# Performance work log

Hardware: AMD Instinct MI355X
Metric: run time of the kernel (lower is better)

Reference implementation:

```python
import jax, jax.numpy as jnp
import numpy as np

K = 128      # num_topics
T = 256      # num_times
E = 320      # rho_size
H = 10       # num_heads (fixed in source)
HD = E // H  # head dim
TM1 = T - 1
EPS = 1e-5   # nn.LayerNorm default eps


def setup_inputs() -> dict:
    key = jax.random.key(0)
    ks = jax.random.split(key, 6)
    s = 0.02
    return {
        "mu_0_alpha": jax.random.normal(ks[0], (1, K, E), jnp.float32),
        "qkv_w": jax.random.normal(ks[1], (3 * E, E), jnp.float32) * s,
        "qkv_b": jnp.zeros((3 * E,), jnp.float32),
        "in_proj_w": jax.random.normal(ks[2], (3 * E, E), jnp.float32) * s,
        "in_proj_b": jnp.zeros((3 * E,), jnp.float32),
        "out_w": jax.random.normal(ks[3], (E, E), jnp.float32) * s,
        "out_b": jnp.zeros((E,), jnp.float32),
        "ln_g": jnp.ones((E,), jnp.float32),
        "ln_b": jnp.zeros((E,), jnp.float32),
    }


def _layer_norm(x, g, b):
    m = jnp.mean(x, axis=-1, keepdims=True)
    v = jnp.mean((x - m) ** 2, axis=-1, keepdims=True)
    return (x - m) * jax.lax.rsqrt(v + EPS) * g + b


def reference(mu_0_alpha, qkv_w, qkv_b, in_proj_w, in_proj_b, out_w, out_b, ln_g, ln_b):
    # nn.MultiheadAttention in-projection split (q/k/v same embed_dim)
    Wq, Wk, Wv = jnp.split(in_proj_w, 3, axis=0)   # each (E, E)
    bq, bk, bv = jnp.split(in_proj_b, 3, axis=0)
    scale = 1.0 / np.sqrt(HD)

    alpha0 = _layer_norm(mu_0_alpha[0], ln_g, ln_b)  # (K, E)
    kc0 = jnp.zeros((TM1 * K, E), jnp.float32)       # persistent projected-K cache
    vc0 = jnp.zeros((TM1 * K, E), jnp.float32)
    pos = jnp.arange(TM1 * K)

    def step(carry, idx):
        alpha, kc, vc = carry
        # per-step qkv_proj (the module's own Linear, before MHA's in-proj)
        qkv = alpha @ qkv_w.T + qkv_b                 # (K, 3E)
        q, k, v = jnp.split(qkv, 3, axis=-1)
        # MHA in-projections; store projected K/V in the cache (equivalent to
        # projecting the concatenated cache each step, since proj is per-row)
        q2 = (q @ Wq.T + bq) * scale                  # (K, E)
        k2 = k @ Wk.T + bk
        v2 = v @ Wv.T + bv
        kc = jax.lax.dynamic_update_slice(kc, k2, (idx * K, 0))
        vc = jax.lax.dynamic_update_slice(vc, v2, (idx * K, 0))
        qh = q2.reshape(K, H, HD).transpose(1, 0, 2)          # (H, K, HD)
        kh = kc.reshape(TM1 * K, H, HD).transpose(1, 0, 2)    # (H, S, HD)
        vh = vc.reshape(TM1 * K, H, HD).transpose(1, 0, 2)
        scores = jnp.einsum('hqd,hkd->hqk', qh, kh)           # (H, K, S)
        valid = pos < (idx + 1) * K                            # growing-KV mask
        scores = jnp.where(valid[None, None, :], scores, -1e30)
        w = jax.nn.softmax(scores, axis=-1)
        o = jnp.einsum('hqk,hkd->hqd', w, vh)                  # (H, K, HD)
        o = o.transpose(1, 0, 2).reshape(K, E) @ out_w.T + out_b
        new_alpha = _layer_norm(o + alpha, ln_g, ln_b)         # residual + LN
        return (new_alpha, kc, vc), new_alpha

    _, alphas_rest = jax.lax.scan(step, (alpha0, kc0, vc0), jnp.arange(TM1))
    return jnp.concatenate([alpha0[None], alphas_rest], axis=0)  # (T, K, E)
```

## Files before the change

kernel.cpp:

```cpp
#include <hip/hip_runtime.h>
#include <hip/hip_bf16.h>
#include <math.h>

typedef __hip_bfloat16 bf16;
using short4v = __attribute__((ext_vector_type(4))) short;
using short8 = __attribute__((ext_vector_type(8))) short;
using f32x4  = __attribute__((ext_vector_type(4))) float;

#define E_ 320
#define K_ 128
#define H_ 10
#define HD_ 32
#define T_ 256
#define TM1_ 255
#define SMAX_ (TM1_*K_)
#define MAXCH_ 30
#define QSCALE 0.17677669529663687f
#define EPS_LN 1e-5f

__device__ __forceinline__ float ldin(const void* p, size_t i, int isbf){
  if (isbf) return __bfloat162float(((const bf16*)p)[i]);
  return ((const float*)p)[i];
}
__device__ __forceinline__ void stout(void* p, size_t i, float v, int isbf){
  if (isbf) ((bf16*)p)[i] = __float2bfloat16(v);
  else      ((float*)p)[i] = v;
}

__device__ __forceinline__ void reduce2_320(float& a, float& b, float* sc){
  #pragma unroll
  for (int off = 32; off > 0; off >>= 1){
    a += __shfl_down(a, off, 64);
    b += __shfl_down(b, off, 64);
  }
  int w = threadIdx.x >> 6, lane = threadIdx.x & 63;
  __syncthreads();
  if (lane == 0){ sc[w] = a; sc[8+w] = b; }
  __syncthreads();
  a = sc[0]+sc[1]+sc[2]+sc[3]+sc[4];
  b = sc[8]+sc[9]+sc[10]+sc[11]+sc[12];
}

__global__ void detect_kernel(const void* __restrict__ mu0, int* __restrict__ flag){
  int lane = threadIdx.x;
  const unsigned short* u = (const unsigned short*)mu0;
  int cnt = 0;
  #pragma unroll
  for (int rep = 0; rep < 2; ++rep){
    unsigned short w = u[(size_t)(lane + rep*64) * 2];
    float v = __uint_as_float(((unsigned int)w) << 16);
    float a = fabsf(v);
    if (a >= 1e-4f && a <= 64.f) cnt++;
  }
  #pragma unroll
  for (int off = 32; off > 0; off >>= 1) cnt += __shfl_down(cnt, off, 64);
  if (lane == 0) *flag = (cnt >= 64) ? 1 : 0;
}

__global__ __launch_bounds__(256) void setup_wc(const void* __restrict__ inw,
                                                const void* __restrict__ qkvw,
                                                bf16* __restrict__ WcB,
                                                const int* __restrict__ flagp){
  const int isbf = *flagp;
  int sec = blockIdx.z;
  int i = blockIdx.y*16 + threadIdx.y;
  int o = blockIdx.x*16 + threadIdx.x;
  __shared__ float As[16][17];
  __shared__ float Bs[16][17];
  float acc = 0.f;
  for (int mt = 0; mt < E_; mt += 16){
    As[threadIdx.y][threadIdx.x] = ldin(inw, ((size_t)(sec*E_ + blockIdx.x*16 + threadIdx.x))*E_ + mt + threadIdx.y, isbf);
    Bs[threadIdx.y][threadIdx.x] = ldin(qkvw, ((size_t)(sec*E_ + mt + threadIdx.x))*E_ + blockIdx.y*16 + threadIdx.y, isbf);
    __syncthreads();
    #pragma unroll
    for (int mm = 0; mm < 16; ++mm) acc += Bs[threadIdx.y][mm] * As[mm][threadIdx.x];
    __syncthreads();
  }
  if (sec == 0) acc *= QSCALE;
  WcB[((size_t)(sec*E_ + o))*E_ + i] = __float2bfloat16(acc);
}

__global__ __launch_bounds__(256) void setup_misc(const void* __restrict__ inw,
                                                  const void* __restrict__ inb,
                                                  const void* __restrict__ qkvb,
                                                  const void* __restrict__ outw,
                                                  const void* __restrict__ outb,
                                                  const void* __restrict__ lng,
                                                  const void* __restrict__ lnb,
                                                  float* __restrict__ bc,
                                                  bf16* __restrict__ owB,
                                                  float* __restrict__ vec,
                                                  const int* __restrict__ flagp){
  const int isbf = *flagp;
  int id = blockIdx.x*256 + threadIdx.x;
  if (id < 960){
    int sec = id / E_, o = id % E_;
    float acc = 0.f;
    for (int m = 0; m < E_; ++m)
      acc += ldin(inw, ((size_t)(sec*E_+o))*E_ + m, isbf) * ldin(qkvb, sec*E_ + m, isbf);
    acc += ldin(inb, id, isbf);
    if (sec == 0) acc *= QSCALE;
    bc[id] = acc;
  }
  int j = id - 1024;
  if (j >= 0 && j < E_*E_){
    owB[j] = __float2bfloat16(ldin(outw, j, isbf));
  }
  int v = id - (1024 + E_*E_);
  if (v >= 0 && v < 960){
    if (v < 320)       vec[v] = ldin(outb, v, isbf);
    else if (v < 640)  vec[v] = ldin(lng, v - 320, isbf);
    else               vec[v] = ldin(lnb, v - 640, isbf);
  }
}

__global__ __launch_bounds__(320) void ln0_kernel(const void* __restrict__ mu0,
                                                  const float* __restrict__ vec,
                                                  float* __restrict__ alpha,
                                                  void* __restrict__ out,
                                                  const int* __restrict__ flagp){
  const int isbf = *flagp;
  int r = blockIdx.x, c = threadIdx.x;
  __shared__ float sc[16];
  float x = ldin(mu0, (size_t)r*E_ + c, isbf);
  float s = x, s2 = x*x;
  reduce2_320(s, s2, sc);
  float mean = s * (1.f/E_);
  float var  = s2 * (1.f/E_) - mean*mean;
  float y = (x - mean) * rsqrtf(var + EPS_LN) * vec[320 + c] + vec[640 + c];
  alpha[(size_t)r*E_ + c] = y;
  stout(out, (size_t)r*E_ + c, y, isbf);
}

__global__ __launch_bounds__(512) void cp_kernel(const float* __restrict__ part,
                                                 const bf16* __restrict__ owB,
                                                 const bf16* __restrict__ WcB,
                                                 const float* __restrict__ bc,
                                                 const float* __restrict__ vec,
                                                 const float* __restrict__ ain,
                                                 float* __restrict__ aout,
                                                 void* __restrict__ out,
                                                 const int* __restrict__ flagp,
                                                 bf16* __restrict__ q2b,
                                                 bf16* __restrict__ kcb,
                                                 bf16* __restrict__ vtb,
                                                 int t, int nch, int do_combine, int do_project){
  const int isbf = *flagp;
  int cg = blockIdx.x;
  int rg = blockIdx.y;
  int r0 = rg*16;
  int tid = threadIdx.x;
  int w = tid >> 6, lane = tid & 63, cn = lane & 15, quad = lane >> 4;

  __shared__ bf16  af[16][328];
  __shared__ float xbuf[16][328];
  __shared__ bf16  a2[16][328];
  __shared__ float mlw[16][10][MAXCH_];
  __shared__ float mlL[16][10];

  if (do_combine){
    if (tid < 160){
      int r = tid / 10, h = tid % 10;
      float mst = -INFINITY;
      for (int ci = 0; ci < nch; ++ci)
        mst = fmaxf(mst, part[(((size_t)h*MAXCH_ + ci)*K_ + r0 + r)*36 + 32]);
      float L = 0.f;
      for (int ci = 0; ci < nch; ++ci){
        size_t base = (((size_t)h*MAXCH_ + ci)*K_ + r0 + r)*36;
        float wgt = __expf(part[base + 32] - mst);
        mlw[r][h][ci] = wgt;
        L += wgt * part[base + 33];
      }
      mlL[r][h] = L;
    }
    __syncthreads();
    for (int v = tid; v < 16*E_; v += 512){
      int r = v / E_, e = v % E_;
      int h = e >> 5, d = e & 31;
      float acc = 0.f;
      for (int ci = 0; ci < nch; ++ci)
        acc += mlw[r][h][ci] * part[(((size_t)h*MAXCH_ + ci)*K_ + r0 + r)*36 + d];
      af[r][e] = __float2bfloat16(acc / mlL[r][h]);
    }
    __syncthreads();

    {
      f32x4 acc[3]; int ntv[3]; int ntc = 0;
      for (int nt = w; nt < 20; nt += 8){ ntv[ntc] = nt; acc[ntc] = (f32x4){0.f,0.f,0.f,0.f}; ntc++; }
      for (int kk = 0; kk < 10; ++kk){
        short8 afr = *(const short8*)(const void*)(&af[cn][kk*32 + quad*8]);
        for (int i = 0; i < ntc; ++i){
          short8 bfr = *(const short8*)(const void*)(owB + ((size_t)(ntv[i]*16 + cn))*E_ + kk*32 + quad*8);
          acc[i] = __builtin_amdgcn_mfma_f32_16x16x32_bf16(afr, bfr, acc[i], 0, 0, 0);
        }
      }
      for (int i = 0; i < ntc; ++i){
        int col = ntv[i]*16 + cn;
        #pragma unroll
        for (int rr = 0; rr < 4; ++rr){
          int lr = quad*4 + rr;
          xbuf[lr][col] = acc[i][rr] + vec[col] + ain[(size_t)(r0+lr)*E_ + col];
        }
      }
    }
    __syncthreads();

    {
      int lr = tid >> 5;
      int j32 = tid & 31;
      float s = 0.f, s2 = 0.f;
      for (int c = j32; c < E_; c += 32){ float x = xbuf[lr][c]; s += x; s2 += x*x; }
      #pragma unroll
      for (int off = 1; off < 32; off <<= 1){
        s  += __shfl_xor(s, off, 32);
        s2 += __shfl_xor(s2, off, 32);
      }
      float mean = s * (1.f/E_);
      float var  = s2 * (1.f/E_) - mean*mean;
      float rs = rsqrtf(var + EPS_LN);
      for (int c = j32; c < E_; c += 32){
        float y = (xbuf[lr][c] - mean) * rs * vec[320 + c] + vec[640 + c];
        a2[lr][c] = __float2bfloat16(y);
        if (cg == 0){
          aout[(size_t)(r0+lr)*E_ + c] = y;
          stout(out, ((size_t)t*K_ + r0 + lr)*E_ + c, y, isbf);
        }
      }
    }
    __syncthreads();
  } else {
    for (int v = tid; v < 16*E_; v += 512){
      int r = v / E_, e = v % E_;
      a2[r][e] = __float2bfloat16(ain[(size_t)(r0+r)*E_ + e]);
    }
    __syncthreads();
  }

  if (!do_project) return;

  {
    f32x4 acc[3]; int ntv[3]; int ntc = 0;
    for (int nt = w; nt < 20; nt += 8){ ntv[ntc] = nt; acc[ntc] = (f32x4){0.f,0.f,0.f,0.f}; ntc++; }
    for (int kk = 0; kk < 10; ++kk){
      short8 afr = *(const short8*)(const void*)(&a2[cn][kk*32 + quad*8]);
      for (int i = 0; i < ntc; ++i){
        short8 bfr = *(const short8*)(const void*)(WcB + ((size_t)(cg*E_ + ntv[i]*16 + cn))*E_ + kk*32 + quad*8);
        acc[i] = __builtin_amdgcn_mfma_f32_16x16x32_bf16(afr, bfr, acc[i], 0, 0, 0);
      }
    }
    for (int i = 0; i < ntc; ++i){
      int coll = ntv[i]*16 + cn;
      float bias = bc[cg*E_ + coll];
      if (cg == 0){
        #pragma unroll
        for (int rr = 0; rr < 4; ++rr)
          q2b[(size_t)(r0 + quad*4 + rr)*E_ + coll] = __float2bfloat16(acc[i][rr] + bias);
      } else if (cg == 1){
        #pragma unroll
        for (int rr = 0; rr < 4; ++rr)
          kcb[((size_t)(t*K_ + r0 + quad*4 + rr))*E_ + coll] = __float2bfloat16(acc[i][rr] + bias);
      } else {
        union { short4v v; bf16 e[4]; } u;
        #pragma unroll
        for (int rr = 0; rr < 4; ++rr) u.e[rr] = __float2bfloat16(acc[i][rr] + bias);
        *(short4v*)(void*)(vtb + (size_t)coll*SMAX_ + t*K_ + r0 + quad*4) = u.v;
      }
    }
  }
}

__global__ __launch_bounds__(512) void attn_mfma(const bf16* __restrict__ q2b,
                                                 const bf16* __restrict__ kcb,
                                                 const bf16* __restrict__ vtb,
                                                 float* __restrict__ part,
                                                 int S, int chunkS){
  int ci = blockIdx.x, h = blockIdx.y;
  int w    = threadIdx.x >> 6;
  int lane = threadIdx.x & 63;
  int cn   = lane & 15;
  int quad = lane >> 4;
  __shared__ bf16 pbuf[8][16][40];

  int s0 = ci*chunkS, s1 = min(s0 + chunkS, S);

  short8 qf = *(const short8*)(const void*)(q2b + (size_t)(w*16 + cn)*E_ + h*HD_ + quad*8);

  f32x4 accT[2];
  accT[0] = (f32x4){0.f,0.f,0.f,0.f};
  accT[1] = (f32x4){0.f,0.f,0.f,0.f};
  float mcol = -INFINITY, lcol = 0.f;

  for (int sb = s0; sb < s1; sb += 32){
    short8 kf0 = *(const short8*)(const void*)(kcb + (size_t)(sb +      cn)*E_ + h*HD_ + quad*8);
    short8 kf1 = *(const short8*)(const void*)(kcb + (size_t)(sb + 16 + cn)*E_ + h*HD_ + quad*8);
    short8 vf0 = *(const short8*)(const void*)(vtb + (size_t)(h*HD_ +      cn)*SMAX_ + sb + quad*8);
    short8 vf1 = *(const short8*)(const void*)(vtb + (size_t)(h*HD_ + 16 + cn)*SMAX_ + sb + quad*8);
    f32x4 z = (f32x4){0.f,0.f,0.f,0.f};
    f32x4 sT0 = __builtin_amdgcn_mfma_f32_16x16x32_bf16(kf0, qf, z, 0, 0, 0);
    f32x4 sT1 = __builtin_amdgcn_mfma_f32_16x16x32_bf16(kf1, qf, z, 0, 0, 0);

    float mx = fmaxf(fmaxf(fmaxf(sT0[0], sT0[1]), fmaxf(sT0[2], sT0[3])),
                     fmaxf(fmaxf(sT1[0], sT1[1]), fmaxf(sT1[2], sT1[3])));
    mx = fmaxf(mx, __shfl_xor(mx, 16, 64));
    mx = fmaxf(mx, __shfl_xor(mx, 32, 64));
    float mn = fmaxf(mcol, mx);
    float corr = __expf(mcol - mn);
    mcol = mn;

    float p0[4], p1[4];
    #pragma unroll
    for (int r = 0; r < 4; ++r){ p0[r] = __expf(sT0[r] - mn); p1[r] = __expf(sT1[r] - mn); }
    float ps = (p0[0]+p0[1]) + (p0[2]+p0[3]) + (p1[0]+p1[1]) + (p1[2]+p1[3]);
    ps += __shfl_xor(ps, 16, 64);
    ps += __shfl_xor(ps, 32, 64);
    lcol = lcol*corr + ps;
    accT[0] *= corr;
    accT[1] *= corr;

    union { short4v v; bf16 e[4]; } u0, u1;
    #pragma unroll
    for (int r = 0; r < 4; ++r){ u0.e[r] = __float2bfloat16(p0[r]); u1.e[r] = __float2bfloat16(p1[r]); }
    *(short4v*)(void*)(&pbuf[w][cn][quad*4])      = u0.v;
    *(short4v*)(void*)(&pbuf[w][cn][16 + quad*4]) = u1.v;
    asm volatile("s_waitcnt lgkmcnt(0)" ::: "memory");
    short8 pf = *(const short8*)(const void*)(&pbuf[w][cn][quad*8]);
    accT[0] = __builtin_amdgcn_mfma_f32_16x16x32_bf16(vf0, pf, accT[0], 0, 0, 0);
    accT[1] = __builtin_amdgcn_mfma_f32_16x16x32_bf16(vf1, pf, accT[1], 0, 0, 0);
  }

  size_t base = (((size_t)h*MAXCH_ + ci)*K_ + 16*w + cn)*36;
  *(f32x4*)(part + base + quad*4)      = accT[0];
  *(f32x4*)(part + base + 16 + quad*4) = accT[1];
  if (quad == 0){ part[base + 32] = mcol; part[base + 33] = lcol; }
}

extern "C" void kernel_launch(void* const* d_in, const int* in_sizes, int n_in,
                              void* d_out, int out_size, void* d_ws, size_t ws_size,
                              hipStream_t stream){
  const void* mu0  = d_in[0];
  const void* qkvw = d_in[1];
  const void* qkvb = d_in[2];
  const void* inw  = d_in[3];
  const void* inb  = d_in[4];
  const void* outw = d_in[5];
  const void* outb = d_in[6];
  const void* lng  = d_in[7];
  const void* lnb  = d_in[8];
  float* ws = (float*)d_ws;

  const size_t O_WCB    = 0;
  const size_t O_OWB    = 153600;
  const size_t O_BC     = 204800;
  const size_t O_VEC    = 205824;
  const size_t O_ALPHA0 = 206848;
  const size_t O_ALPHA1 = 247808;
  const size_t O_PART   = 288768;
  const size_t O_FLAG   = 1671168;
  const size_t O_Q2     = 1671200;
  const size_t O_KC     = 1691680;
  const size_t O_VT     = 6914080;

  bf16*  WcB   = (bf16*)(ws + O_WCB);
  bf16*  owB   = (bf16*)(ws + O_OWB);
  float* bc    = ws + O_BC;
  float* vec   = ws + O_VEC;
  float* abuf0 = ws + O_ALPHA0;
  float* abuf1 = ws + O_ALPHA1;
  float* part  = ws + O_PART;
  int*   flag  = (int*)(ws + O_FLAG);
  bf16*  q2b   = (bf16*)(ws + O_Q2);
  bf16*  kcb   = (bf16*)(ws + O_KC);
  bf16*  vtb   = (bf16*)(ws + O_VT);

  detect_kernel<<<dim3(1), dim3(64), 0, stream>>>(mu0, flag);
  setup_wc<<<dim3(20,20,3), dim3(16,16), 0, stream>>>(inw, qkvw, WcB, flag);
  setup_misc<<<dim3(408), dim3(256), 0, stream>>>(inw, inb, qkvb, outw, outb, lng, lnb, bc, owB, vec, flag);
  ln0_kernel<<<dim3(128), dim3(320), 0, stream>>>(mu0, vec, abuf0, d_out, flag);

  int nch_prev = 0;
  for (int t = 0; t < TM1_; ++t){
    float* ain  = (t == 0) ? abuf0 : ((t & 1) ? abuf0 : abuf1);
    float* aout = (t & 1) ? abuf1 : abuf0;
    cp_kernel<<<dim3(3,8), dim3(512), 0, stream>>>(part, owB, WcB, bc, vec, ain, aout,
                                                   d_out, flag, q2b, kcb, vtb,
                                                   t, nch_prev, (t > 0) ? 1 : 0, 1);
    int S = (t+1)*K_;
    int nch = (S + 255) / 256; if (nch > MAXCH_) nch = MAXCH_;
    int chunkS = (((S + nch - 1)/nch) + 127) / 128 * 128;
    int nchU = (S + chunkS - 1) / chunkS;
    attn_mfma<<<dim3(nchU, H_), dim3(512), 0, stream>>>(q2b, kcb, vtb, part, S, chunkS);
    nch_prev = nchU;
  }
  {
    int t = TM1_;
    float* ain  = (t & 1) ? abuf0 : abuf1;
    float* aout = (t & 1) ? abuf1 : abuf0;
    cp_kernel<<<dim3(3,8), dim3(512), 0, stream>>>(part, owB, WcB, bc, vec, ain, aout,
                                                   d_out, flag, q2b, kcb, vtb,
                                                   t, nch_prev, 1, 0);
  }
}
```

Before: 21.46 ms.

## Fuse per-step kernels into one persistent kernel with grid barriers

Replaces the roughly 510 per-timestep kernel launches (cp_kernel plus attn_mfma) with one persistent kernel of 256 blocks that loops over timesteps and separates phases with a software grid-wide atomic barrier. Attention chunking is retuned to finer 32-aligned chunks capped at 25, and the combine step is unrolled with multiple accumulators. Shared memory is aliased across phases to cut its footprint. The goal is to remove launch overhead and improve parallelism. It relies on all 256 blocks being co-resident and adds the cost of the barrier spin.

```diff
diff --git a/kernel.cpp b/kernel.cpp
--- a/kernel.cpp
+++ b/kernel.cpp
@@ -14,7 +14,8 @@
 #define T_ 256
 #define TM1_ 255
 #define SMAX_ (TM1_*K_)
-#define MAXCH_ 30
+#define MAXCH_ 25
+#define NBLK_ 256
 #define QSCALE 0.17677669529663687f
 #define EPS_LN 1e-5f
 
@@ -41,7 +42,8 @@
   b = sc[8]+sc[9]+sc[10]+sc[11]+sc[12];
 }
 
-__global__ void detect_kernel(const void* __restrict__ mu0, int* __restrict__ flag){
+__global__ void detect_kernel(const void* __restrict__ mu0, int* __restrict__ flag,
+                              unsigned* bar_cnt, unsigned* bar_gen){
   int lane = threadIdx.x;
   const unsigned short* u = (const unsigned short*)mu0;
   int cnt = 0;
@@ -54,7 +56,11 @@
   }
   #pragma unroll
   for (int off = 32; off > 0; off >>= 1) cnt += __shfl_down(cnt, off, 64);
-  if (lane == 0) *flag = (cnt >= 64) ? 1 : 0;
+  if (lane == 0){
+    *flag = (cnt >= 64) ? 1 : 0;
+    *bar_cnt = 0u;
+    *bar_gen = 0u;
+  }
 }
 
 __global__ __launch_bounds__(256) void setup_wc(const void* __restrict__ inw,
@@ -132,55 +138,104 @@
   stout(out, (size_t)r*E_ + c, y, isbf);
 }
 
-__global__ __launch_bounds__(512) void cp_kernel(const float* __restrict__ part,
-                                                 const bf16* __restrict__ owB,
-                                                 const bf16* __restrict__ WcB,
-                                                 const float* __restrict__ bc,
-                                                 const float* __restrict__ vec,
-                                                 const float* __restrict__ ain,
-                                                 float* __restrict__ aout,
-                                                 void* __restrict__ out,
-                                                 const int* __restrict__ flagp,
-                                                 bf16* __restrict__ q2b,
-                                                 bf16* __restrict__ kcb,
-                                                 bf16* __restrict__ vtb,
-                                                 int t, int nch, int do_combine, int do_project){
-  const int isbf = *flagp;
-  int cg = blockIdx.x;
-  int rg = blockIdx.y;
-  int r0 = rg*16;
+__device__ __forceinline__ void grid_barrier(unsigned* cnt, unsigned* gen){
+  __syncthreads();
+  if (threadIdx.x == 0){
+    __threadfence();
+    unsigned g = __hip_atomic_load(gen, __ATOMIC_RELAXED, __HIP_MEMORY_SCOPE_AGENT);
+    unsigned a = __hip_atomic_fetch_add(cnt, 1u, __ATOMIC_ACQ_REL, __HIP_MEMORY_SCOPE_AGENT);
+    if (a == NBLK_ - 1u){
+      __hip_atomic_store(cnt, 0u, __ATOMIC_RELAXED, __HIP_MEMORY_SCOPE_AGENT);
+      __hip_atomic_fetch_add(gen, 1u, __ATOMIC_RELEASE, __HIP_MEMORY_SCOPE_AGENT);
+    } else {
+      while (__hip_atomic_load(gen, __ATOMIC_ACQUIRE, __HIP_MEMORY_SCOPE_AGENT) == g){
+        __builtin_amdgcn_s_sleep(1);
+      }
+    }
+    __threadfence();
+  }
+  __syncthreads();
+}
+
+#define SM_A2   10496
+#define SM_C    20992
+#define SM_MLL  41984
+#define SM_SIZE 42624
+
+__device__ __forceinline__ void cp_phase(int cg, int rg, int t, int nch,
+                                         int do_combine, int do_project,
+                                         const float* part, const bf16* owB, const bf16* WcB,
+                                         const float* bc, const float* vec,
+                                         const float* ain, float* aout, void* out, int isbf,
+                                         bf16* q2b, bf16* kcb, bf16* vtb, char* smem){
   int tid = threadIdx.x;
   int w = tid >> 6, lane = tid & 63, cn = lane & 15, quad = lane >> 4;
-
-  __shared__ bf16  af[16][328];
-  __shared__ float xbuf[16][328];
-  __shared__ bf16  a2[16][328];
-  __shared__ float mlw[16][10][MAXCH_];
-  __shared__ float mlL[16][10];
+  int r0 = rg*16;
+  bf16 (*af)[328]   = (bf16(*)[328])(smem);
+  bf16 (*a2)[328]   = (bf16(*)[328])(smem + SM_A2);
+  float (*xbuf)[328]= (float(*)[328])(smem + SM_C);
+  float (*mlw)[10][26] = (float(*)[10][26])(smem + SM_C);
+  float (*mlL)[10]  = (float(*)[10])(smem + SM_MLL);
 
   if (do_combine){
     if (tid < 160){
-      int r = tid / 10, h = tid % 10;
-      float mst = -INFINITY;
-      for (int ci = 0; ci < nch; ++ci)
-        mst = fmaxf(mst, part[(((size_t)h*MAXCH_ + ci)*K_ + r0 + r)*36 + 32]);
-      float L = 0.f;
-      for (int ci = 0; ci < nch; ++ci){
-        size_t base = (((size_t)h*MAXCH_ + ci)*K_ + r0 + r)*36;
-        float wgt = __expf(part[base + 32] - mst);
-        mlw[r][h][ci] = wgt;
-        L += wgt * part[base + 33];
-      }
-      mlL[r][h] = L;
-    }
-    __syncthreads();
-    for (int v = tid; v < 16*E_; v += 512){
-      int r = v / E_, e = v % E_;
-      int h = e >> 5, d = e & 31;
-      float acc = 0.f;
-      for (int ci = 0; ci < nch; ++ci)
-        acc += mlw[r][h][ci] * part[(((size_t)h*MAXCH_ + ci)*K_ + r0 + r)*36 + d];
-      af[r][e] = __float2bfloat16(acc / mlL[r][h]);
+      int r = tid / 10, h = tid - 10*(tid/10);
+      const float* pb = part + (((size_t)h*MAXCH_)*K_ + r0 + r)*36 + 32;
+      float m0=-INFINITY,m1=-INFINITY,m2=-INFINITY,m3=-INFINITY;
+      int ci = 0;
+      for (; ci + 4 <= nch; ci += 4){
+        m0 = fmaxf(m0, pb[(ci+0)*4608]);
+        m1 = fmaxf(m1, pb[(ci+1)*4608]);
+        m2 = fmaxf(m2, pb[(ci+2)*4608]);
+        m3 = fmaxf(m3, pb[(ci+3)*4608]);
+      }
+      for (; ci < nch; ++ci) m0 = fmaxf(m0, pb[ci*4608]);
+      float mst = fmaxf(fmaxf(m0,m1), fmaxf(m2,m3));
+      float L0=0.f, L1=0.f, L2=0.f, L3=0.f;
+      ci = 0;
+      for (; ci + 4 <= nch; ci += 4){
+        float2 mlv0 = *(const float2*)(pb + (ci+0)*4608);
+        float2 mlv1 = *(const float2*)(pb + (ci+1)*4608);
+        float2 mlv2 = *(const float2*)(pb + (ci+2)*4608);
+        float2 mlv3 = *(const float2*)(pb + (ci+3)*4608);
+        float w0=__expf(mlv0.x-mst), w1=__expf(mlv1.x-mst), w2=__expf(mlv2.x-mst), w3=__expf(mlv3.x-mst);
+        mlw[r][h][ci+0]=w0; mlw[r][h][ci+1]=w1; mlw[r][h][ci+2]=w2; mlw[r][h][ci+3]=w3;
+        L0 += w0*mlv0.y; L1 += w1*mlv1.y; L2 += w2*mlv2.y; L3 += w3*mlv3.y;
+      }
+      for (; ci < nch; ++ci){
+        float2 mlv = *(const float2*)(pb + ci*4608);
+        float wg = __expf(mlv.x - mst);
+        mlw[r][h][ci] = wg; L0 += wg*mlv.y;
+      }
+      mlL[r][h] = (L0+L1)+(L2+L3);
+    }
+    __syncthreads();
+
+    #pragma unroll
+    for (int k = 0; k < 5; ++k){
+      int e1 = tid + (2*k)*512, e2 = tid + (2*k+1)*512;
+      int r1 = e1/320, c1 = e1 - 320*r1, h1 = c1 >> 5, d1 = c1 & 31;
+      int r2 = e2/320, c2 = e2 - 320*r2, h2 = c2 >> 5, d2 = c2 & 31;
+      const float* p1 = part + (((size_t)h1*MAXCH_)*K_ + r0 + r1)*36 + d1;
+      const float* p2 = part + (((size_t)h2*MAXCH_)*K_ + r0 + r2)*36 + d2;
+      float a0=0.f,a1=0.f,a2_=0.f,a3=0.f,b0=0.f,b1=0.f,b2=0.f,b3=0.f;
+      int ci = 0;
+      for (; ci + 4 <= nch; ci += 4){
+        a0 += mlw[r1][h1][ci+0]*p1[(ci+0)*4608];
+        a1 += mlw[r1][h1][ci+1]*p1[(ci+1)*4608];
+        a2_+= mlw[r1][h1][ci+2]*p1[(ci+2)*4608];
+        a3 += mlw[r1][h1][ci+3]*p1[(ci+3)*4608];
+        b0 += mlw[r2][h2][ci+0]*p2[(ci+0)*4608];
+        b1 += mlw[r2][h2][ci+1]*p2[(ci+1)*4608];
+        b2 += mlw[r2][h2][ci+2]*p2[(ci+2)*4608];
+        b3 += mlw[r2][h2][ci+3]*p2[(ci+3)*4608];
+      }
+      for (; ci < nch; ++ci){
+        a0 += mlw[r1][h1][ci]*p1[ci*4608];
+        b0 += mlw[r2][h2][ci]*p2[ci*4608];
+      }
+      af[r1][c1] = __float2bfloat16(((a0+a1)+(a2_+a3)) / mlL[r1][h1]);
+      af[r2][c2] = __float2bfloat16(((b0+b1)+(b2+b3)) / mlL[r2][h2]);
     }
     __syncthreads();
 
@@ -194,6 +249,7 @@
           acc[i] = __builtin_amdgcn_mfma_f32_16x16x32_bf16(afr, bfr, acc[i], 0, 0, 0);
         }
       }
+      __syncthreads();
       for (int i = 0; i < ntc; ++i){
         int col = ntv[i]*16 + cn;
         #pragma unroll
@@ -230,7 +286,7 @@
     __syncthreads();
   } else {
     for (int v = tid; v < 16*E_; v += 512){
-      int r = v / E_, e = v % E_;
+      int r = v / E_, e = v - E_*(v/E_);
       a2[r][e] = __float2bfloat16(ain[(size_t)(r0+r)*E_ + e]);
     }
     __syncthreads();
@@ -269,17 +325,14 @@
   }
 }
 
-__global__ __launch_bounds__(512) void attn_mfma(const bf16* __restrict__ q2b,
-                                                 const bf16* __restrict__ kcb,
-                                                 const bf16* __restrict__ vtb,
-                                                 float* __restrict__ part,
-                                                 int S, int chunkS){
-  int ci = blockIdx.x, h = blockIdx.y;
+__device__ __forceinline__ void attn_cell(int ci, int h, const bf16* q2b, const bf16* kcb,
+                                          const bf16* vtb, float* part, int S, int chunkS,
+                                          char* smem){
   int w    = threadIdx.x >> 6;
   int lane = threadIdx.x & 63;
   int cn   = lane & 15;
   int quad = lane >> 4;
-  __shared__ bf16 pbuf[8][16][40];
+  bf16 (*pbuf)[40] = (bf16(*)[40])(smem + w*16*40*2);
 
   int s0 = ci*chunkS, s1 = min(s0 + chunkS, S);
 
@@ -320,10 +373,10 @@
     union { short4v v; bf16 e[4]; } u0, u1;
     #pragma unroll
     for (int r = 0; r < 4; ++r){ u0.e[r] = __float2bfloat16(p0[r]); u1.e[r] = __float2bfloat16(p1[r]); }
-    *(short4v*)(void*)(&pbuf[w][cn][quad*4])      = u0.v;
-    *(short4v*)(void*)(&pbuf[w][cn][16 + quad*4]) = u1.v;
+    *(short4v*)(void*)(&pbuf[cn][quad*4])      = u0.v;
+    *(short4v*)(void*)(&pbuf[cn][16 + quad*4]) = u1.v;
     asm volatile("s_waitcnt lgkmcnt(0)" ::: "memory");
-    short8 pf = *(const short8*)(const void*)(&pbuf[w][cn][quad*8]);
+    short8 pf = *(const short8*)(const void*)(&pbuf[cn][quad*8]);
     accT[0] = __builtin_amdgcn_mfma_f32_16x16x32_bf16(vf0, pf, accT[0], 0, 0, 0);
     accT[1] = __builtin_amdgcn_mfma_f32_16x16x32_bf16(vf1, pf, accT[1], 0, 0, 0);
   }
@@ -332,6 +385,44 @@
   *(f32x4*)(part + base + quad*4)      = accT[0];
   *(f32x4*)(part + base + 16 + quad*4) = accT[1];
   if (quad == 0){ part[base + 32] = mcol; part[base + 33] = lcol; }
+}
+
+__global__ __launch_bounds__(512) void mega_kernel(const bf16* WcB, const bf16* owB,
+                                                   const float* bc, const float* vec,
+                                                   float* abuf0, float* abuf1,
+                                                   float* part, const int* flagp,
+                                                   bf16* q2b, bf16* kcb, bf16* vtb,
+                                                   void* out,
+                                                   unsigned* bar_cnt, unsigned* bar_gen){
+  __shared__ __align__(16) char smem[SM_SIZE];
+  const int isbf = *flagp;
+  int b = blockIdx.x;
+  int cg = b / 8, rg = b - 8*(b/8);
+
+  int nch_prev = 0;
+  for (int t = 0; t < TM1_; ++t){
+    const float* ain = (t == 0) ? abuf0 : ((t & 1) ? abuf0 : abuf1);
+    float* aout = (t & 1) ? abuf1 : abuf0;
+    if (b < 24)
+      cp_phase(cg, rg, t, nch_prev, (t > 0) ? 1 : 0, 1,
+               part, owB, WcB, bc, vec, ain, aout, out, isbf, q2b, kcb, vtb, smem);
+    grid_barrier(bar_cnt, bar_gen);
+
+    int S = (t+1)*K_;
+    int nch = (S + 127) / 128; if (nch > MAXCH_) nch = MAXCH_;
+    int chunkS = (((S + nch - 1)/nch) + 31) / 32 * 32;
+    int nchU = (S + chunkS - 1) / chunkS;
+    if (b < nchU*10)
+      attn_cell(b/10, b - 10*(b/10), q2b, kcb, vtb, part, S, chunkS, smem);
+    grid_barrier(bar_cnt, bar_gen);
+    nch_prev = nchU;
+  }
+  if (b < 8){
+    const float* ain = abuf0;
+    float* aout = abuf1;
+    cp_phase(0, b, TM1_, nch_prev, 1, 0,
+             part, owB, WcB, bc, vec, ain, aout, out, isbf, q2b, kcb, vtb, smem);
+  }
 }
 
 extern "C" void kernel_launch(void* const* d_in, const int* in_sizes, int n_in,
@@ -352,51 +443,33 @@
   const size_t O_OWB    = 153600;
   const size_t O_BC     = 204800;
   const size_t O_VEC    = 205824;
-  const size_t O_ALPHA0 = 206848;
-  const size_t O_ALPHA1 = 247808;
+  const size_t O_A0     = 206848;
+  const size_t O_A1     = 247808;
   const size_t O_PART   = 288768;
-  const size_t O_FLAG   = 1671168;
-  const size_t O_Q2     = 1671200;
-  const size_t O_KC     = 1691680;
-  const size_t O_VT     = 6914080;
+  const size_t O_FLAG   = 1440768;
+  const size_t O_Q2     = 1440864;
+  const size_t O_KC     = 1461344;
+  const size_t O_VT     = 6683744;
 
   bf16*  WcB   = (bf16*)(ws + O_WCB);
   bf16*  owB   = (bf16*)(ws + O_OWB);
   float* bc    = ws + O_BC;
   float* vec   = ws + O_VEC;
-  float* abuf0 = ws + O_ALPHA0;
-  float* abuf1 = ws + O_ALPHA1;
+  float* abuf0 = ws + O_A0;
+  float* abuf1 = ws + O_A1;
   float* part  = ws + O_PART;
   int*   flag  = (int*)(ws + O_FLAG);
+  unsigned* bar_cnt = (unsigned*)(ws + O_FLAG + 32);
+  unsigned* bar_gen = (unsigned*)(ws + O_FLAG + 64);
   bf16*  q2b   = (bf16*)(ws + O_Q2);
   bf16*  kcb   = (bf16*)(ws + O_KC);
   bf16*  vtb   = (bf16*)(ws + O_VT);
 
-  detect_kernel<<<dim3(1), dim3(64), 0, stream>>>(mu0, flag);
+  detect_kernel<<<dim3(1), dim3(64), 0, stream>>>(mu0, flag, bar_cnt, bar_gen);
   setup_wc<<<dim3(20,20,3), dim3(16,16), 0, stream>>>(inw, qkvw, WcB, flag);
   setup_misc<<<dim3(408), dim3(256), 0, stream>>>(inw, inb, qkvb, outw, outb, lng, lnb, bc, owB, vec, flag);
   ln0_kernel<<<dim3(128), dim3(320), 0, stream>>>(mu0, vec, abuf0, d_out, flag);
-
-  int nch_prev = 0;
-  for (int t = 0; t < TM1_; ++t){
-    float* ain  = (t == 0) ? abuf0 : ((t & 1) ? abuf0 : abuf1);
-    float* aout = (t & 1) ? abuf1 : abuf0;
-    cp_kernel<<<dim3(3,8), dim3(512), 0, stream>>>(part, owB, WcB, bc, vec, ain, aout,
-                                                   d_out, flag, q2b, kcb, vtb,
-                                                   t, nch_prev, (t > 0) ? 1 : 0, 1);
-    int S = (t+1)*K_;
-    int nch = (S + 255) / 256; if (nch > MAXCH_) nch = MAXCH_;
-    int chunkS = (((S + nch - 1)/nch) + 127) / 128 * 128;
-    int nchU = (S + chunkS - 1) / chunkS;
-    attn_mfma<<<dim3(nchU, H_), dim3(512), 0, stream>>>(q2b, kcb, vtb, part, S, chunkS);
-    nch_prev = nchU;
-  }
-  {
-    int t = TM1_;
-    float* ain  = (t & 1) ? abuf0 : abuf1;
-    float* aout = (t & 1) ? abuf1 : abuf0;
-    cp_kernel<<<dim3(3,8), dim3(512), 0, stream>>>(part, owB, WcB, bc, vec, ain, aout,
-                                                   d_out, flag, q2b, kcb, vtb,
-                                                   t, nch_prev, 1, 0);
-  }
-}
+  mega_kernel<<<dim3(NBLK_), dim3(512), 0, stream>>>(WcB, owB, bc, vec, abuf0, abuf1,
+                                                     part, flag, q2b, kcb, vtb, d_out,
+                                                     bar_cnt, bar_gen);
+}
```

After: 85.29 ms. +297.5%, slower.
